# Optimization experiments

Measured on AMD Instinct MI355X. Metric: run time of the kernel, lower is better.

The kernel has to match this reference:

```python
import jax, jax.numpy as jnp
import numpy as np

NUM_USERS = 50000
NUM_ITEMS = 50000
EMB_K = 8
N = 8192
GAMMA = 0.1


def setup_inputs() -> dict:
    key = jax.random.key(0)
    ks = jax.random.split(key, 11)
    s = 1.0
    return {
        "x": jax.random.randint(ks[0], (N, 2), 0, NUM_ITEMS, dtype=jnp.int64) if jax.config.jax_enable_x64 else jax.random.randint(ks[0], (N, 2), 0, NUM_ITEMS),
        "y": jax.random.randint(ks[1], (N, 2), 0, NUM_ITEMS),
        "W": jax.random.normal(ks[2], (NUM_USERS, EMB_K), jnp.float32) * s,
        "H": jax.random.normal(ks[3], (NUM_ITEMS, EMB_K), jnp.float32) * s,
        "ncf_user_emb": jax.random.normal(ks[4], (NUM_USERS, EMB_K), jnp.float32) * s,
        "ncf_item_emb": jax.random.normal(ks[5], (NUM_ITEMS, EMB_K), jnp.float32) * s,
        "lin1_w": jax.random.normal(ks[6], (EMB_K, 2 * EMB_K), jnp.float32) * 0.1,
        "lin1_b": jax.random.normal(ks[7], (EMB_K,), jnp.float32) * 0.1,
        "lin2_w": jax.random.normal(ks[8], (1, EMB_K), jnp.float32) * 0.1,
        "mf_user_emb": jax.random.normal(ks[9], (NUM_USERS, EMB_K), jnp.float32) * s,
        "mf_item_emb": jax.random.normal(ks[10], (NUM_ITEMS, EMB_K), jnp.float32) * s,
    }


def _get_embedding(idx, Wt, Ht):
    # concat user/item embeddings -> [N, 2k], then the (buggy, faithful) min/max step
    feat = jnp.concatenate([Wt[idx[:, 0]], Ht[idx[:, 1]]], axis=1)
    f_min = jnp.min(feat)
    f_max = jnp.max(feat)
    feat = feat - f_min / (f_max - f_min)  # scalar division binds first, as in source
    return feat / feat.shape[1]


def _exp_kernel(X, Y, gamma):
    # Euclidean cdist(Y, X) via gram trick (no [Ny,Nx,d] intermediate), then exp(-d*gamma)
    d2 = (jnp.sum(Y * Y, axis=1)[:, None]
          + jnp.sum(X * X, axis=1)[None, :]
          - 2.0 * (Y @ X.T))
    d = jnp.sqrt(jnp.maximum(d2, 0.0))
    return jnp.exp(-d * gamma)


def reference(x, y, W, H, ncf_user_emb, ncf_item_emb, lin1_w, lin1_b, lin2_w, mf_user_emb, mf_item_emb):
    # kernel branch
    fx = _get_embedding(x, W, H)  # [N, 2k]
    fy = _get_embedding(y, W, H)  # [N, 2k]
    K = _exp_kernel(fx, fy, GAMMA)  # [Ny, Nx]
    # NCF prediction model on x
    ue = ncf_user_emb[x[:, 0]]
    ie = ncf_item_emb[x[:, 1]]
    z = jnp.concatenate([ue, ie], axis=1)
    h1 = jax.nn.relu(z @ lin1_w.T + lin1_b)
    pred = h1 @ lin2_w.T  # [N, 1]
    # MF weight model on x
    mu = mf_user_emb[x[:, 0]]
    mi = mf_item_emb[x[:, 1]]
    w = jnp.sum(mu * mi, axis=1, keepdims=True)  # [N, 1]
    return (K, pred, w)
```

## Files before the change

### kernel.cpp

```cpp
#include <hip/hip_runtime.h>

#define NN 8192
#define GAMMA 0.1f

typedef float v2f __attribute__((ext_vector_type(2)));
typedef float v4f __attribute__((ext_vector_type(4)));

__global__ __launch_bounds__(256) void prep_kernel(
    const int* __restrict__ x, const int* __restrict__ y,
    const float* __restrict__ W, const float* __restrict__ H,
    const float* __restrict__ nue, const float* __restrict__ nie,
    const float* __restrict__ l1w, const float* __restrict__ l1b,
    const float* __restrict__ l2w,
    const float* __restrict__ mfu, const float* __restrict__ mfi,
    float* __restrict__ pred, float* __restrict__ wout,
    float* __restrict__ pmn, float* __restrict__ pmx,
    float* __restrict__ fraw)
{
    int gid = blockIdx.x * 256 + threadIdx.x;
    bool isx = gid < NN;
    int i = isx ? gid : gid - NN;
    const int* idx = isx ? x : y;
    int iu = idx[2 * i], iv = idx[2 * i + 1];

    const float4* wp = (const float4*)(W + (size_t)iu * 8);
    float4 w0 = wp[0], w1 = wp[1];
    const float4* hp = (const float4*)(H + (size_t)iv * 8);
    float4 h0 = hp[0], h1 = hp[1];

    float f[16];
    f[0] = w0.x; f[1] = w0.y; f[2] = w0.z; f[3] = w0.w;
    f[4] = w1.x; f[5] = w1.y; f[6] = w1.z; f[7] = w1.w;
    f[8] = h0.x; f[9] = h0.y; f[10] = h0.z; f[11] = h0.w;
    f[12] = h1.x; f[13] = h1.y; f[14] = h1.z; f[15] = h1.w;

    float4* fr = (float4*)(fraw + (size_t)gid * 16);
    fr[0] = w0; fr[1] = w1; fr[2] = h0; fr[3] = h1;

    float mn = f[0], mx = f[0];
#pragma unroll
    for (int k = 1; k < 16; k++) { mn = fminf(mn, f[k]); mx = fmaxf(mx, f[k]); }
#pragma unroll
    for (int off = 1; off < 64; off <<= 1) {
        mn = fminf(mn, __shfl_xor(mn, off));
        mx = fmaxf(mx, __shfl_xor(mx, off));
    }
    if ((threadIdx.x & 63) == 0) {
        int wid = gid >> 6;
        pmn[wid] = mn;
        pmx[wid] = mx;
    }

    if (isx) {
        const float4* up = (const float4*)(nue + (size_t)iu * 8);
        float4 u0 = up[0], u1 = up[1];
        const float4* ip = (const float4*)(nie + (size_t)iv * 8);
        float4 i0 = ip[0], i1 = ip[1];
        float z[16];
        z[0] = u0.x; z[1] = u0.y; z[2] = u0.z; z[3] = u0.w;
        z[4] = u1.x; z[5] = u1.y; z[6] = u1.z; z[7] = u1.w;
        z[8] = i0.x; z[9] = i0.y; z[10] = i0.z; z[11] = i0.w;
        z[12] = i1.x; z[13] = i1.y; z[14] = i1.z; z[15] = i1.w;

        float p = 0.f;
#pragma unroll
        for (int k = 0; k < 8; k++) {
            float h = l1b[k];
#pragma unroll
            for (int m = 0; m < 16; m++) h = fmaf(z[m], l1w[k * 16 + m], h);
            h = fmaxf(h, 0.f);
            p = fmaf(h, l2w[k], p);
        }
        pred[i] = p;

        const float4* ap = (const float4*)(mfu + (size_t)iu * 8);
        float4 a0 = ap[0], a1 = ap[1];
        const float4* bp = (const float4*)(mfi + (size_t)iv * 8);
        float4 b0 = bp[0], b1 = bp[1];
        float wv = a0.x * b0.x + a0.y * b0.y + a0.z * b0.z + a0.w * b0.w
                 + a1.x * b1.x + a1.y * b1.y + a1.z * b1.z + a1.w * b1.w;
        wout[i] = wv;
    }
}

__global__ __launch_bounds__(256) void norm_kernel(
    const float* __restrict__ fraw,
    const float* __restrict__ pmn, const float* __restrict__ pmx,
    float* __restrict__ fxs, float* __restrict__ fyn,
    float* __restrict__ nx, float* __restrict__ ny)
{
    __shared__ float red[256];
    int tid = threadIdx.x;
    int gid = blockIdx.x * 256 + tid;
    bool isx = gid < NN;
    int side = isx ? 0 : 1;
    const float CC = 2.0813689894397856e-2f;

    if (tid < 128) red[tid] = pmn[side * 128 + tid];
    else           red[tid] = pmx[side * 128 + (tid - 128)];
    __syncthreads();
#pragma unroll
    for (int s = 64; s >= 1; s >>= 1) {
        if ((tid & 127) < s) {
            float o = red[tid + s];
            red[tid] = (tid < 128) ? fminf(red[tid], o) : fmaxf(red[tid], o);
        }
        __syncthreads();
    }
    float fmn = red[0], fmx = red[128];
    float c = fmn / (fmx - fmn);

    int i = isx ? gid : gid - NN;
    const float4* fr = (const float4*)(fraw + (size_t)gid * 16);
    float4 w0 = fr[0], w1 = fr[1], h0 = fr[2], h1 = fr[3];

    float f[16];
    f[0] = w0.x; f[1] = w0.y; f[2] = w0.z; f[3] = w0.w;
    f[4] = w1.x; f[5] = w1.y; f[6] = w1.z; f[7] = w1.w;
    f[8] = h0.x; f[9] = h0.y; f[10] = h0.z; f[11] = h0.w;
    f[12] = h1.x; f[13] = h1.y; f[14] = h1.z; f[15] = h1.w;

    float g[16], o[16];
    float s = 0.f;
    float sc2 = isx ? -2.f : CC;
#pragma unroll
    for (int k = 0; k < 16; k++) {
        g[k] = (f[k] - c) * (1.f / 16.f);
        s = fmaf(g[k], g[k], s);
        o[k] = g[k] * sc2;
    }
    float* dst = (isx ? fxs : fyn) + (size_t)i * 16;
    float4* dv = (float4*)dst;
    dv[0] = make_float4(o[0], o[1], o[2], o[3]);
    dv[1] = make_float4(o[4], o[5], o[6], o[7]);
    dv[2] = make_float4(o[8], o[9], o[10], o[11]);
    dv[3] = make_float4(o[12], o[13], o[14], o[15]);
    (isx ? nx : ny)[i] = s * CC;
}

__global__ __launch_bounds__(256) void kexp_kernel(
    const float* __restrict__ fxs, const float* __restrict__ fyn,
    const float* __restrict__ nx, const float* __restrict__ ny,
    float* __restrict__ K)
{
    __shared__ float sfy[512];
    __shared__ float sny[32];
    int tid = threadIdx.x;
    int ib = blockIdx.y * 32;
    int jb = blockIdx.x * 1024;

    for (int t = tid; t < 512; t += 256) sfy[t] = fyn[(size_t)ib * 16 + t];
    if (tid < 32) sny[tid] = ny[ib + tid];
    __syncthreads();

    int j0 = jb + tid * 4;
    v2f a[4][8];
    float nxr[4];
#pragma unroll
    for (int c2 = 0; c2 < 4; c2++) {
        const float4* p = (const float4*)(fxs + (size_t)(j0 + c2) * 16);
        float4 v0 = p[0], v1 = p[1], v2 = p[2], v3 = p[3];
        a[c2][0] = (v2f){v0.x, v0.y}; a[c2][1] = (v2f){v0.z, v0.w};
        a[c2][2] = (v2f){v1.x, v1.y}; a[c2][3] = (v2f){v1.z, v1.w};
        a[c2][4] = (v2f){v2.x, v2.y}; a[c2][5] = (v2f){v2.z, v2.w};
        a[c2][6] = (v2f){v3.x, v3.y}; a[c2][7] = (v2f){v3.z, v3.w};
        nxr[c2] = nx[j0 + c2];
    }

    const float4* sfy4 = (const float4*)sfy;

#pragma unroll 2
    for (int i = 0; i < 32; i++) {
        float4 q0 = sfy4[i * 4 + 0], q1 = sfy4[i * 4 + 1];
        float4 q2 = sfy4[i * 4 + 2], q3 = sfy4[i * 4 + 3];
        v2f fy[8];
        fy[0] = (v2f){q0.x, q0.y}; fy[1] = (v2f){q0.z, q0.w};
        fy[2] = (v2f){q1.x, q1.y}; fy[3] = (v2f){q1.z, q1.w};
        fy[4] = (v2f){q2.x, q2.y}; fy[5] = (v2f){q2.z, q2.w};
        fy[6] = (v2f){q3.x, q3.y}; fy[7] = (v2f){q3.z, q3.w};
        float nyv = sny[i];
        float r[4];
#pragma unroll
        for (int c2 = 0; c2 < 4; c2++) {
            v2f acc = (v2f){nyv + nxr[c2], 0.f};
#pragma unroll
            for (int k = 0; k < 8; k++)
                acc = __builtin_elementwise_fma(a[c2][k], fy[k], acc);
            float d2 = fmaxf(acc.x + acc.y, 0.f);
            r[c2] = __builtin_amdgcn_exp2f(-__builtin_amdgcn_sqrtf(d2));
        }
        v4f o = (v4f){r[0], r[1], r[2], r[3]};
        __builtin_nontemporal_store(o, (v4f*)(K + (size_t)(ib + i) * NN + j0));
    }
}

extern "C" void kernel_launch(void* const* d_in, const int* in_sizes, int n_in,
                              void* d_out, int out_size, void* d_ws, size_t ws_size,
                              hipStream_t stream) {
    const int* x = (const int*)d_in[0];
    const int* y = (const int*)d_in[1];
    const float* W = (const float*)d_in[2];
    const float* H = (const float*)d_in[3];
    const float* nue = (const float*)d_in[4];
    const float* nie = (const float*)d_in[5];
    const float* l1w = (const float*)d_in[6];
    const float* l1b = (const float*)d_in[7];
    const float* l2w = (const float*)d_in[8];
    const float* mfu = (const float*)d_in[9];
    const float* mfi = (const float*)d_in[10];

    float* out = (float*)d_out;
    float* K = out;
    float* pred = out + (size_t)NN * NN;
    float* wout = pred + NN;

    float* pmn  = (float*)d_ws;
    float* pmx  = pmn + 256;
    float* fraw = pmx + 256;
    float* fxs  = fraw + (size_t)2 * NN * 16;
    float* fyn  = fxs + (size_t)NN * 16;
    float* nx   = fyn + (size_t)NN * 16;
    float* ny   = nx + NN;

    hipLaunchKernelGGL(prep_kernel, dim3(64), dim3(256), 0, stream,
                       x, y, W, H, nue, nie, l1w, l1b, l2w, mfu, mfi, pred, wout,
                       pmn, pmx, fraw);
    hipLaunchKernelGGL(norm_kernel, dim3(64), dim3(256), 0, stream,
                       fraw, pmn, pmx, fxs, fyn, nx, ny);
    hipLaunchKernelGGL(kexp_kernel, dim3(8, 256), dim3(256), 0, stream,
                       fxs, fyn, nx, ny, K);
}
```

Before: 59.24 us.

## Fold min/max normalization algebraically into distance kernel, drop norm pass

Removes the separate normalization kernel by writing pre-scaled raw features plus per-row sum-of-squares and sum from the prep kernel. The distance kernel now reduces the per-wave min/max partials itself and applies the shift through an algebraic correction to the row norms. This saves one launch and the raw-feature round trip through memory. It also doubles the rows per block (64 instead of 32), halving the grid. The cost is an extra reduction in every block and a different floating-point order, which could change rounding when the shift is large.

```diff
diff --git a/kernel.cpp b/kernel.cpp
--- a/kernel.cpp
+++ b/kernel.cpp
@@ -5,6 +5,9 @@
 
 typedef float v2f __attribute__((ext_vector_type(2)));
 typedef float v4f __attribute__((ext_vector_type(4)));
+
+#define CCONST 2.0813689894397856e-2f
+#define CC256  8.130347615003068e-5f
 
 __global__ __launch_bounds__(256) void prep_kernel(
     const int* __restrict__ x, const int* __restrict__ y,
@@ -15,7 +18,8 @@
     const float* __restrict__ mfu, const float* __restrict__ mfi,
     float* __restrict__ pred, float* __restrict__ wout,
     float* __restrict__ pmn, float* __restrict__ pmx,
-    float* __restrict__ fraw)
+    float* __restrict__ fxs, float* __restrict__ fyn,
+    float2* __restrict__ qsx, float2* __restrict__ qsy)
 {
     int gid = blockIdx.x * 256 + threadIdx.x;
     bool isx = gid < NN;
@@ -34,12 +38,14 @@
     f[8] = h0.x; f[9] = h0.y; f[10] = h0.z; f[11] = h0.w;
     f[12] = h1.x; f[13] = h1.y; f[14] = h1.z; f[15] = h1.w;
 
-    float4* fr = (float4*)(fraw + (size_t)gid * 16);
-    fr[0] = w0; fr[1] = w1; fr[2] = h0; fr[3] = h1;
-
     float mn = f[0], mx = f[0];
-#pragma unroll
-    for (int k = 1; k < 16; k++) { mn = fminf(mn, f[k]); mx = fmaxf(mx, f[k]); }
+    float q = 0.f, s = 0.f;
+#pragma unroll
+    for (int k = 0; k < 16; k++) {
+        if (k) { mn = fminf(mn, f[k]); mx = fmaxf(mx, f[k]); }
+        q = fmaf(f[k], f[k], q);
+        s += f[k];
+    }
 #pragma unroll
     for (int off = 1; off < 64; off <<= 1) {
         mn = fminf(mn, __shfl_xor(mn, off));
@@ -50,6 +56,17 @@
         pmn[wid] = mn;
         pmx[wid] = mx;
     }
+
+    float sc = isx ? (-1.f / 8.f) : (CCONST / 16.f);
+    float o[16];
+#pragma unroll
+    for (int k = 0; k < 16; k++) o[k] = f[k] * sc;
+    float4* dv = (float4*)((isx ? fxs : fyn) + (size_t)i * 16);
+    dv[0] = make_float4(o[0], o[1], o[2], o[3]);
+    dv[1] = make_float4(o[4], o[5], o[6], o[7]);
+    dv[2] = make_float4(o[8], o[9], o[10], o[11]);
+    dv[3] = make_float4(o[12], o[13], o[14], o[15]);
+    (isx ? qsx : qsy)[i] = make_float2(q * CC256, s * CC256);
 
     if (isx) {
         const float4* up = (const float4*)(nue + (size_t)iu * 8);
@@ -83,75 +100,44 @@
     }
 }
 
-__global__ __launch_bounds__(256) void norm_kernel(
-    const float* __restrict__ fraw,
-    const float* __restrict__ pmn, const float* __restrict__ pmx,
-    float* __restrict__ fxs, float* __restrict__ fyn,
-    float* __restrict__ nx, float* __restrict__ ny)
-{
-    __shared__ float red[256];
-    int tid = threadIdx.x;
-    int gid = blockIdx.x * 256 + tid;
-    bool isx = gid < NN;
-    int side = isx ? 0 : 1;
-    const float CC = 2.0813689894397856e-2f;
-
-    if (tid < 128) red[tid] = pmn[side * 128 + tid];
-    else           red[tid] = pmx[side * 128 + (tid - 128)];
-    __syncthreads();
-#pragma unroll
-    for (int s = 64; s >= 1; s >>= 1) {
-        if ((tid & 127) < s) {
-            float o = red[tid + s];
-            red[tid] = (tid < 128) ? fminf(red[tid], o) : fmaxf(red[tid], o);
-        }
-        __syncthreads();
-    }
-    float fmn = red[0], fmx = red[128];
-    float c = fmn / (fmx - fmn);
-
-    int i = isx ? gid : gid - NN;
-    const float4* fr = (const float4*)(fraw + (size_t)gid * 16);
-    float4 w0 = fr[0], w1 = fr[1], h0 = fr[2], h1 = fr[3];
-
-    float f[16];
-    f[0] = w0.x; f[1] = w0.y; f[2] = w0.z; f[3] = w0.w;
-    f[4] = w1.x; f[5] = w1.y; f[6] = w1.z; f[7] = w1.w;
-    f[8] = h0.x; f[9] = h0.y; f[10] = h0.z; f[11] = h0.w;
-    f[12] = h1.x; f[13] = h1.y; f[14] = h1.z; f[15] = h1.w;
-
-    float g[16], o[16];
-    float s = 0.f;
-    float sc2 = isx ? -2.f : CC;
-#pragma unroll
-    for (int k = 0; k < 16; k++) {
-        g[k] = (f[k] - c) * (1.f / 16.f);
-        s = fmaf(g[k], g[k], s);
-        o[k] = g[k] * sc2;
-    }
-    float* dst = (isx ? fxs : fyn) + (size_t)i * 16;
-    float4* dv = (float4*)dst;
-    dv[0] = make_float4(o[0], o[1], o[2], o[3]);
-    dv[1] = make_float4(o[4], o[5], o[6], o[7]);
-    dv[2] = make_float4(o[8], o[9], o[10], o[11]);
-    dv[3] = make_float4(o[12], o[13], o[14], o[15]);
-    (isx ? nx : ny)[i] = s * CC;
-}
-
 __global__ __launch_bounds__(256) void kexp_kernel(
     const float* __restrict__ fxs, const float* __restrict__ fyn,
-    const float* __restrict__ nx, const float* __restrict__ ny,
+    const float2* __restrict__ qsx, const float2* __restrict__ qsy,
+    const float* __restrict__ pmn, const float* __restrict__ pmx,
     float* __restrict__ K)
 {
-    __shared__ float sfy[512];
-    __shared__ float sny[32];
+    __shared__ float sfy[1024];
+    __shared__ float sny[64];
+    __shared__ float sred[4];
     int tid = threadIdx.x;
-    int ib = blockIdx.y * 32;
+    int ib = blockIdx.y * 64;
     int jb = blockIdx.x * 1024;
 
-    for (int t = tid; t < 512; t += 256) sfy[t] = fyn[(size_t)ib * 16 + t];
-    if (tid < 32) sny[tid] = ny[ib + tid];
+    {
+        int wv = tid >> 6, ln = tid & 63;
+        const float* psrc = (wv & 1) ? pmx : pmn;
+        int base = (wv >> 1) * 128;
+        float u0 = psrc[base + ln], u1 = psrc[base + ln + 64];
+        float v = (wv & 1) ? fmaxf(u0, u1) : fminf(u0, u1);
+#pragma unroll
+        for (int off = 1; off < 64; off <<= 1) {
+            float o = __shfl_xor(v, off);
+            v = (wv & 1) ? fmaxf(v, o) : fminf(v, o);
+        }
+        if (ln == 0) sred[wv] = v;
+    }
     __syncthreads();
+    float cx = sred[0] / (sred[1] - sred[0]);
+    float cy = sred[2] / (sred[3] - sred[2]);
+    float dl = cy - cx;
+    float e8 = 8.f * CC256 * dl * dl;
+    float dl2 = 2.f * dl;
+
+    for (int t = tid; t < 1024; t += 256) sfy[t] = fyn[(size_t)ib * 16 + t];
+    if (tid < 64) {
+        float2 qs = qsy[ib + tid];
+        sny[tid] = qs.x - dl2 * qs.y + e8;
+    }
 
     int j0 = jb + tid * 4;
     v2f a[4][8];
@@ -164,13 +150,15 @@
         a[c2][2] = (v2f){v1.x, v1.y}; a[c2][3] = (v2f){v1.z, v1.w};
         a[c2][4] = (v2f){v2.x, v2.y}; a[c2][5] = (v2f){v2.z, v2.w};
         a[c2][6] = (v2f){v3.x, v3.y}; a[c2][7] = (v2f){v3.z, v3.w};
-        nxr[c2] = nx[j0 + c2];
-    }
+        float2 qs = qsx[j0 + c2];
+        nxr[c2] = qs.x + dl2 * qs.y + e8;
+    }
+    __syncthreads();
 
     const float4* sfy4 = (const float4*)sfy;
 
 #pragma unroll 2
-    for (int i = 0; i < 32; i++) {
+    for (int i = 0; i < 64; i++) {
         float4 q0 = sfy4[i * 4 + 0], q1 = sfy4[i * 4 + 1];
         float4 q2 = sfy4[i * 4 + 2], q3 = sfy4[i * 4 + 3];
         v2f fy[8];
@@ -182,7 +170,7 @@
         float r[4];
 #pragma unroll
         for (int c2 = 0; c2 < 4; c2++) {
-            v2f acc = (v2f){nyv + nxr[c2], 0.f};
+            v2f acc = (v2f){nyv, nxr[c2]};
 #pragma unroll
             for (int k = 0; k < 8; k++)
                 acc = __builtin_elementwise_fma(a[c2][k], fy[k], acc);
@@ -216,17 +204,14 @@
 
     float* pmn  = (float*)d_ws;
     float* pmx  = pmn + 256;
-    float* fraw = pmx + 256;
-    float* fxs  = fraw + (size_t)2 * NN * 16;
+    float* fxs  = pmx + 256;
     float* fyn  = fxs + (size_t)NN * 16;
-    float* nx   = fyn + (size_t)NN * 16;
-    float* ny   = nx + NN;
+    float2* qsx = (float2*)(fyn + (size_t)NN * 16);
+    float2* qsy = qsx + NN;
 
     hipLaunchKernelGGL(prep_kernel, dim3(64), dim3(256), 0, stream,
                        x, y, W, H, nue, nie, l1w, l1b, l2w, mfu, mfi, pred, wout,
-                       pmn, pmx, fraw);
-    hipLaunchKernelGGL(norm_kernel, dim3(64), dim3(256), 0, stream,
-                       fraw, pmn, pmx, fxs, fyn, nx, ny);
-    hipLaunchKernelGGL(kexp_kernel, dim3(8, 256), dim3(256), 0, stream,
-                       fxs, fyn, nx, ny, K);
+                       pmn, pmx, fxs, fyn, qsx, qsy);
+    hipLaunchKernelGGL(kexp_kernel, dim3(8, 128), dim3(256), 0, stream,
+                       fxs, fyn, qsx, qsy, pmn, pmx, K);
 }
```

Result: slower. 65.90 us (+11.2%).
